# Optimization experiments

Measured on AMD Instinct MI355X. Metric: run time of the kernel, lower is better.

## Reference

```python
import jax, jax.numpy as jnp
import numpy as np

N_NODES = 10000
N_EDGES = 160000
DIM = 1024


def setup_inputs() -> dict:
    key = jax.random.key(0)
    k1, k2, k3 = jax.random.split(key, 3)
    x = jax.random.normal(k1, (N_NODES, DIM), dtype=jnp.float32)
    edge_index = jax.random.randint(k2, (2, N_EDGES), 0, N_NODES, dtype=jnp.int64)
    # Glorot-style init for the GCNConv weight; zero bias (PyG default)
    W = jax.random.normal(k3, (DIM, DIM), dtype=jnp.float32) * (1.0 / np.sqrt(DIM))
    b = jnp.zeros((DIM,), dtype=jnp.float32)
    return {"x": x, "edge_index": edge_index, "W": W, "b": b}


def reference(x, edge_index, W, b):
    """GCNConv (add_self_loops=True, symmetric norm) -> Dropout(eval=identity) -> ReLU."""
    n = x.shape[0]
    loops = jnp.arange(n, dtype=edge_index.dtype)
    src = jnp.concatenate([edge_index[0], loops])  # [E+N]
    dst = jnp.concatenate([edge_index[1], loops])  # [E+N]

    # symmetric normalization: deg^{-1/2}[src] * deg^{-1/2}[dst], deg on dst side
    deg = jax.ops.segment_sum(jnp.ones_like(dst, dtype=x.dtype), dst, num_segments=n)
    dinv = jnp.where(deg > 0, jax.lax.rsqrt(deg), jnp.zeros_like(deg))
    norm = dinv[src] * dinv[dst]  # [E+N]

    h = x @ W                                   # [N, D] dense transform first
    msg = h[src] * norm[:, None]                # gather + edge scaling [E+N, D]
    out = jax.ops.segment_sum(msg, dst, num_segments=n) + b  # scatter-add + bias

    # Dropout(0.5) is identity in eval mode; activation is ReLU
    return jax.nn.relu(out)
```

## Files before the change

### kernel.cpp

```cpp
#include <hip/hip_runtime.h>
#include <hip/hip_bf16.h>
#include <cstdint>
#include <cstddef>

typedef __bf16 bf16x8 __attribute__((ext_vector_type(8)));
typedef __bf16 bf16x4 __attribute__((ext_vector_type(4)));
typedef float  f32x4  __attribute__((ext_vector_type(4)));
typedef float  f32x2  __attribute__((ext_vector_type(2)));

#define D_DIM 1024
#define BM 128
#define BN 128
#define BK 64
#define NXCD 8

#define GLB(p) ((const __attribute__((address_space(1))) void*)(p))
#define LDS(p) ((__attribute__((address_space(3))) void*)(p))

__global__ __launch_bounds__(256) void conv_x_kernel(
    const float* __restrict__ x, __bf16* __restrict__ xb,
    int* __restrict__ cnt, int N, int MP)
{
    int i = blockIdx.x * 256 + threadIdx.x;
    if (i < N) cnt[i] = 0;
    int total = MP * (D_DIM / 8);
    if (i >= total) return;
    int row = i >> 7;
    size_t base = (size_t)i * 8;
    bf16x8 o;
    if (row < N) {
        float4 v0 = *(const float4*)(x + base);
        float4 v1 = *(const float4*)(x + base + 4);
        o[0] = (__bf16)v0.x; o[1] = (__bf16)v0.y; o[2] = (__bf16)v0.z; o[3] = (__bf16)v0.w;
        o[4] = (__bf16)v1.x; o[5] = (__bf16)v1.y; o[6] = (__bf16)v1.z; o[7] = (__bf16)v1.w;
    } else {
        #pragma unroll
        for (int j = 0; j < 8; ++j) o[j] = (__bf16)0.f;
    }
    *(bf16x8*)(xb + base) = o;
}

__global__ void transpose_w_kernel(const float* __restrict__ W, __bf16* __restrict__ wT)
{
    __shared__ float tile[32][33];
    int nb = blockIdx.x * 32, kb = blockIdx.y * 32;
    int tx = threadIdx.x, ty = threadIdx.y;
    #pragma unroll
    for (int i = 0; i < 32; i += 8)
        tile[ty + i][tx] = W[(size_t)(kb + ty + i) * D_DIM + nb + tx];
    __syncthreads();
    #pragma unroll
    for (int i = 0; i < 32; i += 8)
        wT[(size_t)(nb + ty + i) * D_DIM + kb + tx] = (__bf16)tile[tx][ty + i];
}

__global__ __launch_bounds__(256) void count_kernel(
    const int* __restrict__ dst, int* __restrict__ cnt, int E)
{
    int e = blockIdx.x * 256 + threadIdx.x;
    if (e < E) atomicAdd(&cnt[dst[e]], 1);
}

__global__ __launch_bounds__(1024) void scan_kernel(
    const int* __restrict__ cnt, int* __restrict__ row_ptr,
    int* __restrict__ cursor, float* __restrict__ dinv, int N)
{
    __shared__ int sbuf[10240];
    __shared__ int wsum[16];
    __shared__ int sctot;
    int tid = threadIdx.x, lane = tid & 63, wid = tid >> 6;
    int chunks = (N + 1023) >> 10;
    #pragma unroll 4
    for (int ch = 0; ch < chunks; ++ch) {
        int i = (ch << 10) + tid;
        sbuf[(ch << 10) + tid] = (i < N) ? cnt[i] : 0;
    }
    __syncthreads();
    int carry = 0;
    for (int ch = 0; ch < chunks; ++ch) {
        int i = (ch << 10) + tid;
        int c = sbuf[(ch << 10) + tid];
        int p = (c + 7) & ~7;
        int v = p;
        #pragma unroll
        for (int off = 1; off < 64; off <<= 1) {
            int t = __shfl_up(v, off);
            if (lane >= off) v += t;
        }
        if (lane == 63) wsum[wid] = v;
        __syncthreads();
        if (tid < 16) {
            int s = wsum[tid];
            int sv = s;
            #pragma unroll
            for (int off = 1; off < 16; off <<= 1) {
                int t = __shfl_up(sv, off);
                if (tid >= off) sv += t;
            }
            wsum[tid] = sv - s;
            if (tid == 15) sctot = sv;
        }
        __syncthreads();
        int incl = carry + wsum[wid] + v;
        if (i < N) {
            int excl = incl - p;
            row_ptr[i] = excl;
            cursor[i]  = excl;
            dinv[i] = rsqrtf((float)c + 1.0f);
        }
        carry += sctot;
        __syncthreads();
    }
    if (tid == 0) row_ptr[N] = carry;
}

__global__ __launch_bounds__(256) void fill_kernel(
    const int* __restrict__ src, const int* __restrict__ dst,
    int* __restrict__ cursor, int* __restrict__ col, int E)
{
    int e = blockIdx.x * 256 + threadIdx.x;
    if (e < E) {
        int d = dst[e];
        int pos = atomicAdd(&cursor[d], 1);
        col[pos] = src[e] << 11;
    }
}

__global__ __launch_bounds__(256) void pad_fill_kernel(
    const int* __restrict__ cursor, const int* __restrict__ row_ptr,
    int* __restrict__ col, int N)
{
    int d = blockIdx.x * 256 + threadIdx.x;
    if (d >= N) return;
    int zoff = N << 11;
    int p1 = row_ptr[d + 1];
    for (int p = cursor[d]; p < p1; ++p) col[p] = zoff;
}

__global__ __launch_bounds__(256) void gemm_kernel(
    const __bf16* __restrict__ A,
    const __bf16* __restrict__ BT,
    __bf16* __restrict__ C,
    const float* __restrict__ dinv, int Nn,
    int K, int N, int mtiles, int ntiles, int chunk)
{
    __shared__ __bf16 As0[BM * BK], Bs0[BN * BK];
    __shared__ __bf16 As1[BM * BK], Bs1[BN * BK];

    int wg = blockIdx.x;
    int c8 = wg & (NXCD - 1);
    int r  = wg >> 3;
    int bm = c8 * chunk + r / ntiles;
    int bn = r % ntiles;
    if (bm >= mtiles) return;

    int tid = threadIdx.x;
    int wid = tid >> 6, lane = tid & 63;
    int wr = wid >> 1, wc = wid & 1;

    auto stage = [&](int ks, __bf16* dA, __bf16* dB) {
        #pragma unroll
        for (int i = 0; i < 4; ++i) {
            int c   = i * 256 + wid * 64 + lane;
            int row = c >> 3;
            int js  = (c & 7) ^ (row & 7);
            const __bf16* ga = A  + (size_t)(bm * BM + row) * K + ks * BK + js * 8;
            const __bf16* gb = BT + (size_t)(bn * BN + row) * K + ks * BK + js * 8;
            __builtin_amdgcn_global_load_lds(GLB(ga), LDS(dA + c * 8), 16, 0, 0);
            __builtin_amdgcn_global_load_lds(GLB(gb), LDS(dB + c * 8), 16, 0, 0);
        }
    };

    f32x4 acc[4][4] = {};
    const int ksteps = K / BK;

    __bf16 *rdA = As0, *rdB = Bs0, *wrA = As1, *wrB = Bs1;
    stage(0, rdA, rdB);
    asm volatile("s_waitcnt vmcnt(0)" ::: "memory");
    __syncthreads();

    for (int ks = 0; ks < ksteps; ++ks) {
        if (ks + 1 < ksteps) stage(ks + 1, wrA, wrB);
        #pragma unroll
        for (int kk = 0; kk < 2; ++kk) {
            bf16x8 af[4], bfr[4];
            int jgrp = kk * 4 + (lane >> 4);
            #pragma unroll
            for (int mi = 0; mi < 4; ++mi) {
                int rr = wr * 64 + mi * 16 + (lane & 15);
                af[mi] = *(const bf16x8*)(rdA + rr * BK + ((jgrp ^ (rr & 7)) << 3));
            }
            #pragma unroll
            for (int ni = 0; ni < 4; ++ni) {
                int rr = wc * 64 + ni * 16 + (lane & 15);
                bfr[ni] = *(const bf16x8*)(rdB + rr * BK + ((jgrp ^ (rr & 7)) << 3));
            }
            #pragma unroll
            for (int mi = 0; mi < 4; ++mi)
                #pragma unroll
                for (int ni = 0; ni < 4; ++ni)
                    acc[mi][ni] = __builtin_amdgcn_mfma_f32_16x16x32_bf16(
                        af[mi], bfr[ni], acc[mi][ni], 0, 0, 0);
        }
        asm volatile("s_waitcnt vmcnt(0)" ::: "memory");
        __syncthreads();
        __bf16* t;
        t = rdA; rdA = wrA; wrA = t;
        t = rdB; rdB = wrB; wrB = t;
    }

    #pragma unroll
    for (int mi = 0; mi < 4; ++mi)
        #pragma unroll
        for (int rr = 0; rr < 4; ++rr) {
            int row = bm * BM + wr * 64 + mi * 16 + (lane >> 4) * 4 + rr;
            float dvr = (row < Nn) ? dinv[row] : 0.0f;
            #pragma unroll
            for (int ni = 0; ni < 4; ++ni) {
                int colc = bn * BN + wc * 64 + ni * 16 + (lane & 15);
                C[(size_t)row * N + colc] = (__bf16)(acc[mi][ni][rr] * dvr);
            }
        }
}

__global__ __launch_bounds__(256) void scatter_kernel(
    const __bf16* __restrict__ h, const int* __restrict__ row_ptr,
    const int* __restrict__ col, const float* __restrict__ dinv,
    const float* __restrict__ b, float* __restrict__ out, int N)
{
    int blk = blockIdx.x;
    int c   = blk & (NXCD - 1);
    int q   = blk >> 3;
    int wid = threadIdx.x >> 6, lane = threadIdx.x & 63;
    int d = q * 4 + wid;
    if (d >= N) return;

    const char* hb = (const char*)h + (size_t)c * 256;
    int lane4 = lane * 4;

    uint32_t su = *(const uint32_t*)(hb + (((uint32_t)d << 11) + lane4));
    f32x2 a;
    a[0] = __uint_as_float(su << 16);
    a[1] = __uint_as_float(su & 0xffff0000u);

    int r0 = row_ptr[d], r1 = row_ptr[d + 1];
    for (int e = r0; e < r1; e += 8) {
        int off[8];
        #pragma unroll
        for (int t = 0; t < 8; ++t) off[t] = col[e + t];
        uint32_t u[8];
        #pragma unroll
        for (int t = 0; t < 8; ++t)
            u[t] = *(const uint32_t*)(hb + ((uint32_t)off[t] + lane4));
        #pragma unroll
        for (int t = 0; t < 8; ++t) {
            f32x2 v;
            v[0] = __uint_as_float(u[t] << 16);
            v[1] = __uint_as_float(u[t] & 0xffff0000u);
            a += v;
        }
    }

    float dv = dinv[d];
    int cbase = c * 128 + lane * 2;
    f32x2 bb = *(const f32x2*)(b + cbase);
    f32x2 o;
    o[0] = fmaxf(fmaf(a[0], dv, bb[0]), 0.f);
    o[1] = fmaxf(fmaf(a[1], dv, bb[1]), 0.f);
    __builtin_nontemporal_store(o, (f32x2*)(out + (size_t)d * D_DIM + cbase));
}

extern "C" void kernel_launch(void* const* d_in, const int* in_sizes, int n_in,
                              void* d_out, int out_size, void* d_ws, size_t ws_size,
                              hipStream_t stream)
{
    const float* x  = (const float*)d_in[0];
    const int*   ei = (const int*)d_in[1];
    const float* W  = (const float*)d_in[2];
    const float* b  = (const float*)d_in[3];
    float* out = (float*)d_out;

    const int N = in_sizes[0] / D_DIM;
    const int E = in_sizes[1] / 2;
    const int MP = ((N + BM - 1) / BM) * BM;
    const int K = D_DIM;

    const int* src = ei;
    const int* dst = ei + E;

    char* ws = (char*)d_ws;
    size_t off = 0;
    auto alloc = [&](size_t bytes) -> char* {
        char* p = ws + off;
        off += (bytes + 255) & ~(size_t)255;
        return p;
    };
    __bf16* xb     = (__bf16*)alloc((size_t)MP * D_DIM * 2);
    __bf16* wT     = (__bf16*)alloc((size_t)D_DIM * D_DIM * 2);
    __bf16* h      = (__bf16*)alloc((size_t)MP * D_DIM * 2);
    int*    cnt    = (int*)alloc((size_t)N * 4);
    int*    rowptr = (int*)alloc((size_t)(N + 1) * 4);
    int*    cursor = (int*)alloc((size_t)N * 4);
    int*    colbuf = (int*)alloc((size_t)(E + 7 * N + 64) * 4);
    float*  dinv   = (float*)alloc((size_t)N * 4);
    (void)ws_size;

    int groups = MP * (D_DIM / 8);
    conv_x_kernel<<<(groups + 255) / 256, 256, 0, stream>>>(x, xb, cnt, N, MP);
    transpose_w_kernel<<<dim3(D_DIM / 32, D_DIM / 32), dim3(32, 8), 0, stream>>>(W, wT);
    count_kernel<<<(E + 255) / 256, 256, 0, stream>>>(dst, cnt, E);
    scan_kernel<<<1, 1024, 0, stream>>>(cnt, rowptr, cursor, dinv, N);
    fill_kernel<<<(E + 255) / 256, 256, 0, stream>>>(src, dst, cursor, colbuf, E);
    pad_fill_kernel<<<(N + 255) / 256, 256, 0, stream>>>(cursor, rowptr, colbuf, N);
    int mtiles = MP / BM;
    int ntiles = D_DIM / BN;
    int chunk  = (mtiles + NXCD - 1) / NXCD;
    int nblocks = NXCD * chunk * ntiles;
    gemm_kernel<<<nblocks, 256, 0, stream>>>(xb, wT, h, dinv, N, K, D_DIM,
                                             mtiles, ntiles, chunk);
    int sblocks = ((N + 3) / 4) * NXCD;
    scatter_kernel<<<sblocks, 256, 0, stream>>>(h, rowptr, colbuf, dinv, b, out, N);
}
```

Before: 120.5 us.

## Merge prep and fill launches, single-buffer GEMM LDS, vectorize scatter index loads

Fuses the x conversion and W transpose into one launch, and the CSR fill and pad steps into another, so fewer kernels are launched. The pad step now uses row_ptr+cnt instead of the atomically advanced cursor, which removes its ordering dependence on the fill step. The GEMM drops its LDS double buffering in favour of a single buffer with a load-wait-compute loop, halving shared memory but losing the overlap of global loads with MFMA. The scatter kernel loads column indices as two int4 vectors instead of eight scalars.

```diff
diff --git a/kernel.cpp b/kernel.cpp
--- a/kernel.cpp
+++ b/kernel.cpp
@@ -4,7 +4,6 @@
 #include <cstddef>
 
 typedef __bf16 bf16x8 __attribute__((ext_vector_type(8)));
-typedef __bf16 bf16x4 __attribute__((ext_vector_type(4)));
 typedef float  f32x4  __attribute__((ext_vector_type(4)));
 typedef float  f32x2  __attribute__((ext_vector_type(2)));
 
@@ -17,41 +16,43 @@
 #define GLB(p) ((const __attribute__((address_space(1))) void*)(p))
 #define LDS(p) ((__attribute__((address_space(3))) void*)(p))
 
-__global__ __launch_bounds__(256) void conv_x_kernel(
+__global__ __launch_bounds__(256) void prep_kernel(
     const float* __restrict__ x, __bf16* __restrict__ xb,
-    int* __restrict__ cnt, int N, int MP)
-{
-    int i = blockIdx.x * 256 + threadIdx.x;
-    if (i < N) cnt[i] = 0;
-    int total = MP * (D_DIM / 8);
-    if (i >= total) return;
-    int row = i >> 7;
-    size_t base = (size_t)i * 8;
-    bf16x8 o;
-    if (row < N) {
-        float4 v0 = *(const float4*)(x + base);
-        float4 v1 = *(const float4*)(x + base + 4);
-        o[0] = (__bf16)v0.x; o[1] = (__bf16)v0.y; o[2] = (__bf16)v0.z; o[3] = (__bf16)v0.w;
-        o[4] = (__bf16)v1.x; o[5] = (__bf16)v1.y; o[6] = (__bf16)v1.z; o[7] = (__bf16)v1.w;
+    const float* __restrict__ W, __bf16* __restrict__ wT,
+    int* __restrict__ cnt, int N, int MP, int nconv)
+{
+    int blk = blockIdx.x, tid = threadIdx.x;
+    if (blk < nconv) {
+        int i = blk * 256 + tid;
+        if (i < N) cnt[i] = 0;
+        int total = MP * (D_DIM / 8);
+        if (i >= total) return;
+        int row = i >> 7;
+        size_t base = (size_t)i * 8;
+        bf16x8 o;
+        if (row < N) {
+            float4 v0 = *(const float4*)(x + base);
+            float4 v1 = *(const float4*)(x + base + 4);
+            o[0] = (__bf16)v0.x; o[1] = (__bf16)v0.y; o[2] = (__bf16)v0.z; o[3] = (__bf16)v0.w;
+            o[4] = (__bf16)v1.x; o[5] = (__bf16)v1.y; o[6] = (__bf16)v1.z; o[7] = (__bf16)v1.w;
+        } else {
+            #pragma unroll
+            for (int j = 0; j < 8; ++j) o[j] = (__bf16)0.f;
+        }
+        *(bf16x8*)(xb + base) = o;
     } else {
-        #pragma unroll
-        for (int j = 0; j < 8; ++j) o[j] = (__bf16)0.f;
-    }
-    *(bf16x8*)(xb + base) = o;
-}
-
-__global__ void transpose_w_kernel(const float* __restrict__ W, __bf16* __restrict__ wT)
-{
-    __shared__ float tile[32][33];
-    int nb = blockIdx.x * 32, kb = blockIdx.y * 32;
-    int tx = threadIdx.x, ty = threadIdx.y;
-    #pragma unroll
-    for (int i = 0; i < 32; i += 8)
-        tile[ty + i][tx] = W[(size_t)(kb + ty + i) * D_DIM + nb + tx];
-    __syncthreads();
-    #pragma unroll
-    for (int i = 0; i < 32; i += 8)
-        wT[(size_t)(nb + ty + i) * D_DIM + kb + tx] = (__bf16)tile[tx][ty + i];
+        __shared__ float tile[32][33];
+        int bb = blk - nconv;
+        int nb = (bb & 31) * 32, kb = (bb >> 5) * 32;
+        int tx = tid & 31, ty = tid >> 5;
+        #pragma unroll
+        for (int i = 0; i < 32; i += 8)
+            tile[ty + i][tx] = W[(size_t)(kb + ty + i) * D_DIM + nb + tx];
+        __syncthreads();
+        #pragma unroll
+        for (int i = 0; i < 32; i += 8)
+            wT[(size_t)(nb + ty + i) * D_DIM + kb + tx] = (__bf16)tile[tx][ty + i];
+    }
 }
 
 __global__ __launch_bounds__(256) void count_kernel(
@@ -114,27 +115,27 @@
     if (tid == 0) row_ptr[N] = carry;
 }
 
-__global__ __launch_bounds__(256) void fill_kernel(
+__global__ __launch_bounds__(256) void fillpad_kernel(
     const int* __restrict__ src, const int* __restrict__ dst,
-    int* __restrict__ cursor, int* __restrict__ col, int E)
-{
-    int e = blockIdx.x * 256 + threadIdx.x;
-    if (e < E) {
-        int d = dst[e];
-        int pos = atomicAdd(&cursor[d], 1);
-        col[pos] = src[e] << 11;
-    }
-}
-
-__global__ __launch_bounds__(256) void pad_fill_kernel(
-    const int* __restrict__ cursor, const int* __restrict__ row_ptr,
-    int* __restrict__ col, int N)
-{
-    int d = blockIdx.x * 256 + threadIdx.x;
-    if (d >= N) return;
-    int zoff = N << 11;
-    int p1 = row_ptr[d + 1];
-    for (int p = cursor[d]; p < p1; ++p) col[p] = zoff;
+    int* __restrict__ cursor, const int* __restrict__ cnt,
+    const int* __restrict__ row_ptr, int* __restrict__ col,
+    int E, int N, int nfill)
+{
+    int blk = blockIdx.x, tid = threadIdx.x;
+    if (blk < nfill) {
+        int e = blk * 256 + tid;
+        if (e < E) {
+            int d = dst[e];
+            int pos = atomicAdd(&cursor[d], 1);
+            col[pos] = src[e] << 11;
+        }
+    } else {
+        int d = (blk - nfill) * 256 + tid;
+        if (d >= N) return;
+        int zoff = N << 11;
+        int p1 = row_ptr[d + 1];
+        for (int p = row_ptr[d] + cnt[d]; p < p1; ++p) col[p] = zoff;
+    }
 }
 
 __global__ __launch_bounds__(256) void gemm_kernel(
@@ -144,8 +145,8 @@
     const float* __restrict__ dinv, int Nn,
     int K, int N, int mtiles, int ntiles, int chunk)
 {
-    __shared__ __bf16 As0[BM * BK], Bs0[BN * BK];
-    __shared__ __bf16 As1[BM * BK], Bs1[BN * BK];
+    __shared__ __bf16 As[BM * BK];
+    __shared__ __bf16 Bs[BN * BK];
 
     int wg = blockIdx.x;
     int c8 = wg & (NXCD - 1);
@@ -158,7 +159,10 @@
     int wid = tid >> 6, lane = tid & 63;
     int wr = wid >> 1, wc = wid & 1;
 
-    auto stage = [&](int ks, __bf16* dA, __bf16* dB) {
+    f32x4 acc[4][4] = {};
+    const int ksteps = K / BK;
+
+    for (int ks = 0; ks < ksteps; ++ks) {
         #pragma unroll
         for (int i = 0; i < 4; ++i) {
             int c   = i * 256 + wid * 64 + lane;
@@ -166,21 +170,11 @@
             int js  = (c & 7) ^ (row & 7);
             const __bf16* ga = A  + (size_t)(bm * BM + row) * K + ks * BK + js * 8;
             const __bf16* gb = BT + (size_t)(bn * BN + row) * K + ks * BK + js * 8;
-            __builtin_amdgcn_global_load_lds(GLB(ga), LDS(dA + c * 8), 16, 0, 0);
-            __builtin_amdgcn_global_load_lds(GLB(gb), LDS(dB + c * 8), 16, 0, 0);
-        }
-    };
-
-    f32x4 acc[4][4] = {};
-    const int ksteps = K / BK;
-
-    __bf16 *rdA = As0, *rdB = Bs0, *wrA = As1, *wrB = Bs1;
-    stage(0, rdA, rdB);
-    asm volatile("s_waitcnt vmcnt(0)" ::: "memory");
-    __syncthreads();
-
-    for (int ks = 0; ks < ksteps; ++ks) {
-        if (ks + 1 < ksteps) stage(ks + 1, wrA, wrB);
+            __builtin_amdgcn_global_load_lds(GLB(ga), LDS(As + c * 8), 16, 0, 0);
+            __builtin_amdgcn_global_load_lds(GLB(gb), LDS(Bs + c * 8), 16, 0, 0);
+        }
+        asm volatile("s_waitcnt vmcnt(0)" ::: "memory");
+        __syncthreads();
         #pragma unroll
         for (int kk = 0; kk < 2; ++kk) {
             bf16x8 af[4], bfr[4];
@@ -188,12 +182,12 @@
             #pragma unroll
             for (int mi = 0; mi < 4; ++mi) {
                 int rr = wr * 64 + mi * 16 + (lane & 15);
-                af[mi] = *(const bf16x8*)(rdA + rr * BK + ((jgrp ^ (rr & 7)) << 3));
+                af[mi] = *(const bf16x8*)(As + rr * BK + ((jgrp ^ (rr & 7)) << 3));
             }
             #pragma unroll
             for (int ni = 0; ni < 4; ++ni) {
                 int rr = wc * 64 + ni * 16 + (lane & 15);
-                bfr[ni] = *(const bf16x8*)(rdB + rr * BK + ((jgrp ^ (rr & 7)) << 3));
+                bfr[ni] = *(const bf16x8*)(Bs + rr * BK + ((jgrp ^ (rr & 7)) << 3));
             }
             #pragma unroll
             for (int mi = 0; mi < 4; ++mi)
@@ -202,11 +196,7 @@
                     acc[mi][ni] = __builtin_amdgcn_mfma_f32_16x16x32_bf16(
                         af[mi], bfr[ni], acc[mi][ni], 0, 0, 0);
         }
-        asm volatile("s_waitcnt vmcnt(0)" ::: "memory");
-        __syncthreads();
-        __bf16* t;
-        t = rdA; rdA = wrA; wrA = t;
-        t = rdB; rdB = wrB; wrB = t;
+        __syncthreads();
     }
 
     #pragma unroll
@@ -245,13 +235,17 @@
 
     int r0 = row_ptr[d], r1 = row_ptr[d + 1];
     for (int e = r0; e < r1; e += 8) {
-        int off[8];
-        #pragma unroll
-        for (int t = 0; t < 8; ++t) off[t] = col[e + t];
+        int4 c0 = *(const int4*)(col + e);
+        int4 c1 = *(const int4*)(col + e + 4);
         uint32_t u[8];
-        #pragma unroll
-        for (int t = 0; t < 8; ++t)
-            u[t] = *(const uint32_t*)(hb + ((uint32_t)off[t] + lane4));
+        u[0] = *(const uint32_t*)(hb + ((uint32_t)c0.x + lane4));
+        u[1] = *(const uint32_t*)(hb + ((uint32_t)c0.y + lane4));
+        u[2] = *(const uint32_t*)(hb + ((uint32_t)c0.z + lane4));
+        u[3] = *(const uint32_t*)(hb + ((uint32_t)c0.w + lane4));
+        u[4] = *(const uint32_t*)(hb + ((uint32_t)c1.x + lane4));
+        u[5] = *(const uint32_t*)(hb + ((uint32_t)c1.y + lane4));
+        u[6] = *(const uint32_t*)(hb + ((uint32_t)c1.z + lane4));
+        u[7] = *(const uint32_t*)(hb + ((uint32_t)c1.w + lane4));
         #pragma unroll
         for (int t = 0; t < 8; ++t) {
             f32x2 v;
@@ -305,13 +299,15 @@
     float*  dinv   = (float*)alloc((size_t)N * 4);
     (void)ws_size;
 
-    int groups = MP * (D_DIM / 8);
-    conv_x_kernel<<<(groups + 255) / 256, 256, 0, stream>>>(x, xb, cnt, N, MP);
-    transpose_w_kernel<<<dim3(D_DIM / 32, D_DIM / 32), dim3(32, 8), 0, stream>>>(W, wT);
+    int nconv = (MP * (D_DIM / 8) + 255) / 256;
+    int ntr   = (D_DIM / 32) * (D_DIM / 32);
+    prep_kernel<<<nconv + ntr, 256, 0, stream>>>(x, xb, W, wT, cnt, N, MP, nconv);
     count_kernel<<<(E + 255) / 256, 256, 0, stream>>>(dst, cnt, E);
     scan_kernel<<<1, 1024, 0, stream>>>(cnt, rowptr, cursor, dinv, N);
-    fill_kernel<<<(E + 255) / 256, 256, 0, stream>>>(src, dst, cursor, colbuf, E);
-    pad_fill_kernel<<<(N + 255) / 256, 256, 0, stream>>>(cursor, rowptr, colbuf, N);
+    int nfill = (E + 255) / 256;
+    int npad  = (N + 255) / 256;
+    fillpad_kernel<<<nfill + npad, 256, 0, stream>>>(src, dst, cursor, cnt,
+                                                     rowptr, colbuf, E, N, nfill);
     int mtiles = MP / BM;
     int ntiles = D_DIM / BN;
     int chunk  = (mtiles + NXCD - 1) / NXCD;
```

Result: faster. 114.4 us (-5.0%).
